# Performance work log

Measured on AMD Instinct MI355X. Metric: run time of the kernel, lower is better.

Reference implementation:

```python
import jax, jax.numpy as jnp
import numpy as np
import math

T, B, E, H, NEXP = 512, 8, 1024, 32, 256
DH = E // H
S = T + NEXP
SCALING = (DH / 1) ** 0.5 / DH  # = 1/sqrt(head_dim) for d_tilde=1
LN_EPS = 1e-5


def _xavier(key, shape, gain):
    fan_in, fan_out = shape[1], shape[0]
    a = gain * math.sqrt(6.0 / (fan_in + fan_out))
    return jax.random.uniform(key, shape, jnp.float32, -a, a)


def setup_inputs() -> dict:
    key = jax.random.key(0)
    ks = jax.random.split(key, 12)
    g = 1.0 / math.sqrt(2.0)  # xavier gain 1/sqrt(2*d_tilde)
    return {
        "query": jax.random.normal(ks[0], (T, B, E), jnp.float32),
        "attn_bias": jax.random.normal(ks[1], (B * H, T, S), jnp.float32) * 0.1,
        "outcell_index": jax.random.randint(ks[2], (B, NEXP), 0, T - 1),
        "expand_mask": jax.random.randint(ks[3], (B, NEXP), 0, 2).astype(bool),
        "key_padding_mask": jnp.zeros((B, T), bool),
        "Wq": _xavier(ks[4], (E, E), g),
        "bq": jnp.zeros((E,), jnp.float32),
        "Wk": _xavier(ks[5], (E, E), g),  # k_proj has no bias (k_bias=False)
        "Wv": _xavier(ks[6], (E, E), g),
        "bv": jnp.zeros((E,), jnp.float32),
        "Wo": _xavier(ks[7], (E, E), 1.0),
        "bo": jnp.zeros((E,), jnp.float32),
        "ln_g": jnp.ones((E,), jnp.float32),
        "ln_b": jnp.zeros((E,), jnp.float32),
    }


def reference(query, attn_bias, outcell_index, expand_mask, key_padding_mask,
              Wq, bq, Wk, Wv, bv, Wo, bo, ln_g, ln_b):
    # projections (Time x Batch x Channel)
    q = (query @ Wq.T + bq) * SCALING          # [T,B,E]
    k = query @ Wk.T                            # [T,B,E] (no bias)
    v = query @ Wv.T + bv                       # [T,B,E]

    # PBC gather-expansion of K/V along time dim (note +1 offset as in source)
    idx = outcell_index.T + 1                   # [NEXP,B]
    idx3 = jnp.broadcast_to(idx[:, :, None], (NEXP, B, E))
    expand_k = jnp.take_along_axis(k, idx3, axis=0)
    expand_v = jnp.take_along_axis(v, idx3, axis=0)
    k = jnp.concatenate([k, expand_k], axis=0)  # [S,B,E]
    v = jnp.concatenate([v, expand_v], axis=0)  # [S,B,E]

    # split heads
    qh = q.reshape(T, B, H, DH)
    kh = k.reshape(S, B, H, DH)
    vh = v.reshape(S, B, H, DH)

    scores = jnp.einsum("tbhd,sbhd->bhts", qh, kh)  # [B,H,T,S]
    scores = scores + attn_bias.reshape(B, H, T, S)

    mask = jnp.concatenate([key_padding_mask, expand_mask], axis=1)  # [B,S]
    scores = jnp.where(mask[:, None, None, :], -jnp.inf, scores)

    probs = jax.nn.softmax(scores, axis=-1)      # [B,H,T,S]

    attn = jnp.einsum("bhts,sbhd->tbhd", probs, vh).reshape(T, B, E)

    # layer norm then output projection
    mu = attn.mean(-1, keepdims=True)
    var = ((attn - mu) ** 2).mean(-1, keepdims=True)
    attn = (attn - mu) * jax.lax.rsqrt(var + LN_EPS) * ln_g + ln_b
    out = attn @ Wo.T + bo                       # [T,B,E]

    attn_weights_mean = probs.mean(axis=1)       # [B,T,S] (mean over heads)
    return out, attn_weights_mean
```

## Files before the change

### kernel.cpp

```cpp
#include <hip/hip_runtime.h>

#define DEV __device__ __forceinline__

typedef short bh8 __attribute__((ext_vector_type(8)));
typedef short bh4 __attribute__((ext_vector_type(4)));
typedef float fx4 __attribute__((ext_vector_type(4)));

#define T_ 512
#define B_ 8
#define E_ 1024
#define H_ 32
#define DH_ 32
#define S_ 768
#define NEXP_ 256
#define SCALING_ 0.17677669529663687f
#define OFF_QB    ((size_t)0)
#define OFF_WB    ((size_t)8388608)
#define OFF_QRM   ((size_t)16777216)
#define OFF_KRM   ((size_t)25165824)
#define OFF_VRM   ((size_t)33554432)
#define OFF_KBF   ((size_t)41943040)
#define OFF_VT    ((size_t)54525952)
#define OFF_ATTN  ((size_t)67108864)
#define OFF_XHAT  ((size_t)75497472)
#define OFF_MASK  ((size_t)83886080)
#define OFF_FLAG  ((size_t)83910656)

#define BARRIER_LGKM() do { \
  asm volatile("s_waitcnt lgkmcnt(0)" ::: "memory"); \
  __builtin_amdgcn_s_barrier(); \
} while (0)

#define WAIT_VM0_BARRIER() do { \
  asm volatile("s_waitcnt vmcnt(0)" ::: "memory"); \
  __builtin_amdgcn_s_barrier(); \
} while (0)

DEV float bf2f(short u) {
  union { unsigned int i; float f; } x;
  x.i = ((unsigned int)(unsigned short)u) << 16;
  return x.f;
}
DEV short f2bf(float f) {
  union { float f; unsigned int u; } x; x.f = f;
  unsigned int r = x.u + 0x7fffu + ((x.u >> 16) & 1u);
  return (short)(r >> 16);
}
DEV void gl_lds16(const void* g, void* l) {
  __builtin_amdgcn_global_load_lds(
      (const __attribute__((address_space(1))) unsigned int*)g,
      (__attribute__((address_space(3))) unsigned int*)l, 16, 0, 0);
}

__global__ __launch_bounds__(256) void conv_all(
    const float* __restrict__ q, const float* __restrict__ wq,
    const float* __restrict__ wk, const float* __restrict__ wv,
    const float* __restrict__ wo, short* __restrict__ QB, short* __restrict__ WB,
    const unsigned char* __restrict__ em, int* __restrict__ flag) {
  if (blockIdx.x == 0) {
    __shared__ int f;
    if (threadIdx.x == 0) f = 0;
    __syncthreads();
    for (int i = threadIdx.x; i < 2048; i += 256)
      if ((i & 3) && em[i]) atomicOr(&f, 1);
    __syncthreads();
    if (threadIdx.x == 0) *flag = f;
  }
  size_t i4 = ((size_t)blockIdx.x * 256 + threadIdx.x) * 4;
  const float* s; short* d;
  if (i4 < (size_t)4194304) { s = q + i4; d = QB + i4; }
  else {
    size_t r = i4 - 4194304; int m = (int)(r >> 20); size_t o = r & 1048575;
    const float* ws4[4] = {wq, wk, wv, wo};
    s = ws4[m] + o; d = WB + ((size_t)m << 20) + o;
  }
  fx4 v = *(const fx4*)s;
  bh4 p = { f2bf(v[0]), f2bf(v[1]), f2bf(v[2]), f2bf(v[3]) };
  *(bh4*)d = p;
}

__global__ __launch_bounds__(256) void qkv_gemm(
    const short* __restrict__ QB, const short* __restrict__ WB,
    const float* __restrict__ bq, const float* __restrict__ bv,
    short* __restrict__ q_rm, short* __restrict__ k_rm, short* __restrict__ v_rm) {
  __shared__ __align__(16) short As[128 * 32];
  __shared__ __align__(16) short Ws[128 * 32];
  const int tid = threadIdx.x;
  const int mt = blockIdx.x, nt = blockIdx.y;
  const int mat = nt >> 3;
  const size_t m0 = (size_t)mt * 128;
  const int n0 = (nt & 7) << 7;
  const short* W = WB + (size_t)mat * (1024 * 1024);
  const int l = tid & 63, wv_ = tid >> 6;
  const int lt = l & 15, g = l >> 4;
  const int wm = wv_ >> 1, wn = wv_ & 1;
  fx4 acc[4][4];
#pragma unroll
  for (int i = 0; i < 4; ++i)
#pragma unroll
    for (int j = 0; j < 4; ++j) acc[i][j] = fx4{0.f, 0.f, 0.f, 0.f};

  const int r0 = tid >> 2, c0 = tid & 3;
  for (int kt = 0; kt < 32; ++kt) {
    const int k0 = kt * 32;
    __syncthreads();
    gl_lds16(QB + (m0 + r0) * 1024 + k0 + c0 * 8,        As + r0 * 32 + c0 * 8);
    gl_lds16(QB + (m0 + 64 + r0) * 1024 + k0 + c0 * 8,   As + (64 + r0) * 32 + c0 * 8);
    gl_lds16(W + (size_t)(n0 + r0) * 1024 + k0 + c0 * 8,      Ws + r0 * 32 + c0 * 8);
    gl_lds16(W + (size_t)(n0 + 64 + r0) * 1024 + k0 + c0 * 8, Ws + (64 + r0) * 32 + c0 * 8);
    __syncthreads();
    bh8 af[4], wf[4];
#pragma unroll
    for (int i = 0; i < 4; ++i) af[i] = *(const bh8*)(As + (wm * 64 + i * 16 + lt) * 32 + g * 8);
#pragma unroll
    for (int j = 0; j < 4; ++j) wf[j] = *(const bh8*)(Ws + (wn * 64 + j * 16 + lt) * 32 + g * 8);
#pragma unroll
    for (int i = 0; i < 4; ++i)
#pragma unroll
      for (int j = 0; j < 4; ++j)
        acc[i][j] = __builtin_amdgcn_mfma_f32_16x16x32_bf16(af[i], wf[j], acc[i][j], 0, 0, 0);
  }
  short* outp = (mat == 0) ? q_rm : (mat == 1) ? k_rm : v_rm;
#pragma unroll
  for (int i = 0; i < 4; ++i) {
    const size_t rowb = m0 + wm * 64 + i * 16 + g * 4;
#pragma unroll
    for (int j = 0; j < 4; ++j) {
      const int col = n0 + wn * 64 + j * 16 + lt;
      const float bias = (mat == 0) ? bq[col] : (mat == 2) ? bv[col] : 0.0f;
#pragma unroll
      for (int jj = 0; jj < 4; ++jj) {
        float v = acc[i][j][jj] + bias;
        if (mat == 0) v *= SCALING_;
        outp[(rowb + jj) * 1024 + col] = f2bf(v);
      }
    }
  }
}

__global__ __launch_bounds__(256) void repack(
    const short* __restrict__ k_rm, const short* __restrict__ v_rm,
    const int* __restrict__ oc, const unsigned char* __restrict__ em,
    const unsigned char* __restrict__ kp, const int* __restrict__ flag,
    short* __restrict__ kbf, short* __restrict__ vT, float* __restrict__ maskval) {
  __shared__ __align__(16) short lv[2][64 * 40];
  const int bid = blockIdx.x, tid = threadIdx.x;
  if (bid < 768) {
#pragma unroll
    for (int k = 0; k < 4; ++k) {
      int u = bid * 1024 + k * 256 + tid;
      int d8 = u & 3;
      int s = (u >> 2) % 768;
      int hb = (u >> 2) / 768;
      int b = hb >> 5, h = hb & 31;
      int srct = (s < 512) ? s : (oc[b * 256 + (s - 512)] + 1);
      bh8 val = *(const bh8*)(k_rm + ((size_t)srct * 8 + b) * 1024 + h * 32 + d8 * 8);
      *(bh8*)(kbf + ((size_t)hb * 768 + s) * 32 + d8 * 8) = val;
    }
  } else if (bid < 2304) {
    int idx2 = bid - 768;
    int s_loc = tid >> 2, d8 = tid & 3;
#pragma unroll
    for (int k = 0; k < 2; ++k) {
      int chunk = idx2 * 2 + k;
      int c = chunk % 12, hb = chunk / 12;
      int b = hb >> 5, h = hb & 31;
      int s = c * 64 + s_loc;
      int srct = (s < 512) ? s : (oc[b * 256 + (s - 512)] + 1);
      bh8 val = *(const bh8*)(v_rm + ((size_t)srct * 8 + b) * 1024 + h * 32 + d8 * 8);
      *(bh8*)(lv[k] + s_loc * 40 + d8 * 8) = val;
    }
    __syncthreads();
    int d = tid >> 3, sj = tid & 7;
#pragma unroll
    for (int k = 0; k < 2; ++k) {
      int chunk = idx2 * 2 + k;
      int c = chunk % 12, hb = chunk / 12;
      bh8 o;
#pragma unroll
      for (int e = 0; e < 8; ++e) o[e] = lv[k][(sj * 8 + e) * 40 + d];
      *(bh8*)(vT + ((size_t)hb * 32 + d) * 768 + c * 64 + sj * 8) = o;
    }
  } else {
    int u = (bid - 2304) * 256 + tid;
    if (u < 6144) {
      int s = u % 768, b = u / 768;
      int m;
      if (*flag) {
        m = (s < 512) ? (int)kp[b * 512 + s] : (int)em[b * 256 + (s - 512)];
      } else {
        const int* kpi = (const int*)kp; const int* emi = (const int*)em;
        m = (s < 512) ? kpi[b * 512 + s] : emi[b * 256 + (s - 512)];
      }
      maskval[u] = m ? -3.0e38f : 0.0f;
    }
  }
}

__global__ __launch_bounds__(512) void attn_kernel(
    const short* __restrict__ q_rm, const short* __restrict__ kbf,
    const short* __restrict__ vT, const float* __restrict__ bias,
    const float* __restrict__ maskval, short* __restrict__ attn_bf,
    float* __restrict__ mean_out, const float* __restrict__ lg,
    const float* __restrict__ lb, short* __restrict__ xhat) {
  __shared__ __align__(16) float bias_lds[2][16 * 768];
  __shared__ __align__(16) short p_st[8 * 16 * 40];
  __shared__ float lpart[8][16];
  __shared__ __align__(16) float attred[2][8 * 64 * 8];
  __shared__ __align__(16) float maskv[768];

  const int tid = threadIdx.x, blk = blockIdx.x;
  const int tt = blk & 31, b = blk >> 5;
  const int t0 = tt * 16;
  const int w = tid >> 6, l = tid & 63, lt = l & 15, g = l >> 4;
  const int sbase = w * 96;

  for (int u = tid; u < 768; u += 512) maskv[u] = maskval[b * 768 + u];

  const float* bias_base = bias + ((size_t)(b * 32) * 512 + t0) * 768;
#pragma unroll
  for (int r = 0; r < 6; ++r)
    gl_lds16(bias_base + (size_t)(r * 512 + tid) * 4,
             (char*)bias_lds[0] + (size_t)(r * 512 + tid) * 16);
  asm volatile("s_waitcnt lgkmcnt(0) vmcnt(0)" ::: "memory");
  __builtin_amdgcn_s_barrier();

  const fx4 zf = {0.f, 0.f, 0.f, 0.f};
  float msum[24];
#pragma unroll
  for (int i = 0; i < 24; ++i) msum[i] = 0.f;

  for (int hh = 0; hh < 32; ++hh) {
    const int cur = hh & 1;
    const int bh = b * 32 + hh;

    if (hh < 31) {
      const float* nb = bias_base + (size_t)(hh + 1) * 512 * 768;
#pragma unroll
      for (int r = 0; r < 6; ++r)
        gl_lds16(nb + (size_t)(r * 512 + tid) * 4,
                 (char*)bias_lds[cur ^ 1] + (size_t)(r * 512 + tid) * 16);
    }

    const bh8 qf = *(const bh8*)(q_rm + ((size_t)(t0 + lt) * 8 + b) * 1024 + hh * 32 + g * 8);
    const short* kp_ = kbf + (size_t)bh * 768 * 32;

    unsigned exu[12];
    float ls0 = 0.f, ls1 = 0.f, ls2 = 0.f, ls3 = 0.f;
#pragma unroll
    for (int c = 0; c < 6; ++c) {
      const int s0 = sbase + c * 16;
      bh8 kf = *(const bh8*)(kp_ + (s0 + lt) * 32 + g * 8);
      fx4 sc = __builtin_amdgcn_mfma_f32_16x16x32_bf16(qf, kf, zf, 0, 0, 0);
      const float mv = maskv[s0 + lt];
      const float* bl = bias_lds[cur] + (g * 4) * 768 + s0 + lt;
      float e0 = __expf(sc[0] + bl[0]       + mv);
      float e1 = __expf(sc[1] + bl[768]     + mv);
      float e2 = __expf(sc[2] + bl[2 * 768] + mv);
      float e3 = __expf(sc[3] + bl[3 * 768] + mv);
      ls0 += e0; ls1 += e1; ls2 += e2; ls3 += e3;
      exu[c * 2]     = (unsigned)(unsigned short)f2bf(e0) | ((unsigned)(unsigned short)f2bf(e1) << 16);
      exu[c * 2 + 1] = (unsigned)(unsigned short)f2bf(e2) | ((unsigned)(unsigned short)f2bf(e3) << 16);
    }
#pragma unroll
    for (int m = 1; m < 16; m <<= 1) {
      ls0 += __shfl_xor(ls0, m); ls1 += __shfl_xor(ls1, m);
      ls2 += __shfl_xor(ls2, m); ls3 += __shfl_xor(ls3, m);
    }
    if (lt == 0) {
      lpart[w][g * 4 + 0] = ls0; lpart[w][g * 4 + 1] = ls1;
      lpart[w][g * 4 + 2] = ls2; lpart[w][g * 4 + 3] = ls3;
    }
    BARRIER_LGKM();
    float linv[4];
#pragma unroll
    for (int jj = 0; jj < 4; ++jj) {
      float s8v = 0.f;
#pragma unroll
      for (int w2 = 0; w2 < 8; ++w2) s8v += lpart[w2][g * 4 + jj];
      linv[jj] = 1.0f / s8v;
    }
    float sacc = 0.f;
#pragma unroll
    for (int w2 = 0; w2 < 8; ++w2) sacc += lpart[w2][lt];
    const float linv_acc = 1.0f / sacc;

    fx4 acc0 = zf, acc1 = zf;
    const short* vp0 = vT + ((size_t)bh * 32 + lt) * 768;
    const short* vp1 = vp0 + 16 * 768;
    short* pw_base = p_st + w * 640;
#pragma unroll
    for (int c2 = 0; c2 < 3; ++c2) {
      const int s0 = sbase + c2 * 32;
#pragma unroll
      for (int cc = 0; cc < 2; ++cc) {
        const int c = c2 * 2 + cc;
        unsigned u01 = exu[c * 2], u23 = exu[c * 2 + 1];
        short* pcol = pw_base + cc * 16 + lt;
        pcol[(g * 4 + 0) * 40] = (short)(u01 & 0xffffu);
        pcol[(g * 4 + 1) * 40] = (short)(u01 >> 16);
        pcol[(g * 4 + 2) * 40] = (short)(u23 & 0xffffu);
        pcol[(g * 4 + 3) * 40] = (short)(u23 >> 16);
        msum[c * 4 + 0] += bf2f((short)(u01 & 0xffffu)) * linv[0];
        msum[c * 4 + 1] += bf2f((short)(u01 >> 16)) * linv[1];
        msum[c * 4 + 2] += bf2f((short)(u23 & 0xffffu)) * linv[2];
        msum[c * 4 + 3] += bf2f((short)(u23 >> 16)) * linv[3];
      }
      bh8 pf = *(const bh8*)(pw_base + lt * 40 + g * 8);
      bh8 vf0 = *(const bh8*)(vp0 + s0 + g * 8);
      bh8 vf1 = *(const bh8*)(vp1 + s0 + g * 8);
      acc0 = __builtin_amdgcn_mfma_f32_16x16x32_bf16(vf0, pf, acc0, 0, 0, 0);
      acc1 = __builtin_amdgcn_mfma_f32_16x16x32_bf16(vf1, pf, acc1, 0, 0, 0);
    }
#pragma unroll
    for (int jj = 0; jj < 4; ++jj) { acc0[jj] *= linv_acc; acc1[jj] *= linv_acc; }

    float* ar = attred[cur] + (w * 64 + l) * 8;
    *(fx4*)(ar) = acc0;
    *(fx4*)(ar + 4) = acc1;
    BARRIER_LGKM();
    if (w < 2) {
      const float* ab = attred[cur];
      float s0v = 0.f, s1v = 0.f, s2v = 0.f, s3v = 0.f;
#pragma unroll
      for (int w2 = 0; w2 < 8; ++w2) {
        const float* a2 = ab + (w2 * 64 + l) * 8 + w * 4;
        s0v += a2[0]; s1v += a2[1]; s2v += a2[2]; s3v += a2[3];
      }
      bh4 o = { f2bf(s0v), f2bf(s1v), f2bf(s2v), f2bf(s3v) };
      *(bh4*)(attn_bf + ((size_t)(t0 + lt) * 8 + b) * 1024 + hh * 32 + w * 16 + g * 4) = o;
    }
    WAIT_VM0_BARRIER();
  }

#pragma unroll
  for (int r2 = 0; r2 < 2; ++r2) {
    const int trow = t0 + w * 2 + r2;
    const size_t row = (size_t)trow * 8 + b;
    const short* x = attn_bf + row * 1024 + l * 16;
    bh8 a0 = *(const bh8*)x, a1 = *(const bh8*)(x + 8);
    float xs[16];
#pragma unroll
    for (int i = 0; i < 8; ++i) { xs[i] = bf2f(a0[i]); xs[8 + i] = bf2f(a1[i]); }
    float s1 = 0.f, s2 = 0.f;
#pragma unroll
    for (int i = 0; i < 16; ++i) { s1 += xs[i]; s2 += xs[i] * xs[i]; }
    for (int m = 1; m < 64; m <<= 1) { s1 += __shfl_xor(s1, m); s2 += __shfl_xor(s2, m); }
    const float mu = s1 * (1.0f / 1024.0f);
    float var = s2 * (1.0f / 1024.0f) - mu * mu;
    var = fmaxf(var, 0.f);
    const float rs = rsqrtf(var + 1e-5f);
    const float* lgp = lg + l * 16;
    const float* lbp = lb + l * 16;
    bh8 o0, o1;
#pragma unroll
    for (int i = 0; i < 8; ++i) {
      o0[i] = f2bf((xs[i] - mu) * rs * lgp[i] + lbp[i]);
      o1[i] = f2bf((xs[8 + i] - mu) * rs * lgp[8 + i] + lbp[8 + i]);
    }
    short* y = xhat + row * 1024 + l * 16;
    *(bh8*)y = o0;
    *(bh8*)(y + 8) = o1;
  }

  float* mob = mean_out + ((size_t)b * 512 + t0) * 768;
#pragma unroll
  for (int c = 0; c < 6; ++c) {
    const int s = sbase + c * 16 + lt;
#pragma unroll
    for (int jj = 0; jj < 4; ++jj) {
      mob[(size_t)(g * 4 + jj) * 768 + s] = msum[c * 4 + jj] * 0.03125f;
    }
  }
}

__global__ __launch_bounds__(256) void out_gemm(
    const short* __restrict__ XH, const short* __restrict__ WoB,
    const float* __restrict__ bo, float* __restrict__ out) {
  __shared__ __align__(16) short As[128 * 32];
  __shared__ __align__(16) short Ws[128 * 32];
  const int tid = threadIdx.x;
  const int mt = blockIdx.x, nt = blockIdx.y;
  const size_t m0 = (size_t)mt * 128;
  const int n0 = nt << 7;
  const int l = tid & 63, wv_ = tid >> 6;
  const int lt = l & 15, g = l >> 4;
  const int wm = wv_ >> 1, wn = wv_ & 1;
  fx4 acc[4][4];
#pragma unroll
  for (int i = 0; i < 4; ++i)
#pragma unroll
    for (int j = 0; j < 4; ++j) acc[i][j] = fx4{0.f, 0.f, 0.f, 0.f};
  const int r0 = tid >> 2, c0 = tid & 3;
  for (int kt = 0; kt < 32; ++kt) {
    const int k0 = kt * 32;
    __syncthreads();
    gl_lds16(XH + (m0 + r0) * 1024 + k0 + c0 * 8,        As + r0 * 32 + c0 * 8);
    gl_lds16(XH + (m0 + 64 + r0) * 1024 + k0 + c0 * 8,   As + (64 + r0) * 32 + c0 * 8);
    gl_lds16(WoB + (size_t)(n0 + r0) * 1024 + k0 + c0 * 8,      Ws + r0 * 32 + c0 * 8);
    gl_lds16(WoB + (size_t)(n0 + 64 + r0) * 1024 + k0 + c0 * 8, Ws + (64 + r0) * 32 + c0 * 8);
    __syncthreads();
    bh8 af[4], wf[4];
#pragma unroll
    for (int i = 0; i < 4; ++i) af[i] = *(const bh8*)(As + (wm * 64 + i * 16 + lt) * 32 + g * 8);
#pragma unroll
    for (int j = 0; j < 4; ++j) wf[j] = *(const bh8*)(Ws + (wn * 64 + j * 16 + lt) * 32 + g * 8);
#pragma unroll
    for (int i = 0; i < 4; ++i)
#pragma unroll
      for (int j = 0; j < 4; ++j)
        acc[i][j] = __builtin_amdgcn_mfma_f32_16x16x32_bf16(af[i], wf[j], acc[i][j], 0, 0, 0);
  }
#pragma unroll
  for (int i = 0; i < 4; ++i) {
    const size_t rowb = m0 + wm * 64 + i * 16 + g * 4;
#pragma unroll
    for (int j = 0; j < 4; ++j) {
      const int col = n0 + wn * 64 + j * 16 + lt;
      const float bb = bo[col];
#pragma unroll
      for (int jj = 0; jj < 4; ++jj)
        out[(rowb + jj) * 1024 + col] = acc[i][j][jj] + bb;
    }
  }
}

extern "C" void kernel_launch(void* const* d_in, const int* in_sizes, int n_in,
                              void* d_out, int out_size, void* d_ws, size_t ws_size,
                              hipStream_t stream) {
  const float* query = (const float*)d_in[0];
  const float* attn_bias = (const float*)d_in[1];
  const int* oc = (const int*)d_in[2];
  const unsigned char* em = (const unsigned char*)d_in[3];
  const unsigned char* kp = (const unsigned char*)d_in[4];
  const float* Wq = (const float*)d_in[5];
  const float* bq = (const float*)d_in[6];
  const float* Wk = (const float*)d_in[7];
  const float* Wv = (const float*)d_in[8];
  const float* bv = (const float*)d_in[9];
  const float* Wo = (const float*)d_in[10];
  const float* bo = (const float*)d_in[11];
  const float* lg = (const float*)d_in[12];
  const float* lb = (const float*)d_in[13];

  char* w = (char*)d_ws;
  short* QB    = (short*)(w + OFF_QB);
  short* WB    = (short*)(w + OFF_WB);
  short* QRM   = (short*)(w + OFF_QRM);
  short* KRM   = (short*)(w + OFF_KRM);
  short* VRM   = (short*)(w + OFF_VRM);
  short* KBF   = (short*)(w + OFF_KBF);
  short* VT    = (short*)(w + OFF_VT);
  short* ATTN  = (short*)(w + OFF_ATTN);
  short* XHAT  = (short*)(w + OFF_XHAT);
  float* MASK  = (float*)(w + OFF_MASK);
  int*   FLAG  = (int*)(w + OFF_FLAG);

  float* out0 = (float*)d_out;
  float* mean_out = out0 + (size_t)T_ * B_ * E_;

  conv_all<<<8192, 256, 0, stream>>>(query, Wq, Wk, Wv, Wo, QB, WB, em, FLAG);
  qkv_gemm<<<dim3(32, 24), 256, 0, stream>>>(QB, WB, bq, bv, QRM, KRM, VRM);
  repack<<<2328, 256, 0, stream>>>(KRM, VRM, oc, em, kp, FLAG, KBF, VT, MASK);
  attn_kernel<<<256, 512, 0, stream>>>(QRM, KBF, VT, attn_bias, MASK, ATTN,
                                       mean_out, lg, lb, XHAT);
  out_gemm<<<dim3(32, 8), 256, 0, stream>>>(XHAT, WB + (size_t)3 * 1024 * 1024, bo, out0);
}
```

Baseline: 262.7 us.

## Split attention heads across two blocks, halve LDS, add mean-reduce and LN kernels

The attention kernel now launches 512 blocks, each covering 16 of the 32 heads, so it uses more CUs. Bias is single-buffered with a synchronous load per head, which cuts LDS use so several blocks fit per CU. The per-head mean is written as two partial slabs that a new kernel adds together, and LayerNorm moves into its own kernel. The cost is that bias prefetch no longer overlaps compute, there is extra global traffic for the partial means, and two more kernels are launched.

```diff
diff --git a/kernel.cpp b/kernel.cpp
--- a/kernel.cpp
+++ b/kernel.cpp
@@ -25,6 +25,8 @@
 #define OFF_XHAT  ((size_t)75497472)
 #define OFF_MASK  ((size_t)83886080)
 #define OFF_FLAG  ((size_t)83910656)
+#define OFF_MEANP ((size_t)100663296)
+#define SLAB_ ((size_t)B_ * T_ * S_)
 
 #define BARRIER_LGKM() do { \
   asm volatile("s_waitcnt lgkmcnt(0)" ::: "memory"); \
@@ -32,7 +34,7 @@
 } while (0)
 
 #define WAIT_VM0_BARRIER() do { \
-  asm volatile("s_waitcnt vmcnt(0)" ::: "memory"); \
+  asm volatile("s_waitcnt vmcnt(0) lgkmcnt(0)" ::: "memory"); \
   __builtin_amdgcn_s_barrier(); \
 } while (0)
 
@@ -197,50 +199,42 @@
   }
 }
 
-__global__ __launch_bounds__(512) void attn_kernel(
+__global__ __launch_bounds__(512, 4) void attn_kernel(
     const short* __restrict__ q_rm, const short* __restrict__ kbf,
     const short* __restrict__ vT, const float* __restrict__ bias,
     const float* __restrict__ maskval, short* __restrict__ attn_bf,
-    float* __restrict__ mean_out, const float* __restrict__ lg,
-    const float* __restrict__ lb, short* __restrict__ xhat) {
-  __shared__ __align__(16) float bias_lds[2][16 * 768];
+    float* __restrict__ mean_part) {
+  __shared__ __align__(16) float bias_lds[16 * 768];
   __shared__ __align__(16) short p_st[8 * 16 * 40];
   __shared__ float lpart[8][16];
-  __shared__ __align__(16) float attred[2][8 * 64 * 8];
+  __shared__ __align__(16) float attred[8 * 64 * 8];
   __shared__ __align__(16) float maskv[768];
 
   const int tid = threadIdx.x, blk = blockIdx.x;
-  const int tt = blk & 31, b = blk >> 5;
+  const int hg = blk & 1, tt = (blk >> 1) & 31, b = blk >> 6;
   const int t0 = tt * 16;
   const int w = tid >> 6, l = tid & 63, lt = l & 15, g = l >> 4;
   const int sbase = w * 96;
 
   for (int u = tid; u < 768; u += 512) maskv[u] = maskval[b * 768 + u];
+  BARRIER_LGKM();
 
   const float* bias_base = bias + ((size_t)(b * 32) * 512 + t0) * 768;
-#pragma unroll
-  for (int r = 0; r < 6; ++r)
-    gl_lds16(bias_base + (size_t)(r * 512 + tid) * 4,
-             (char*)bias_lds[0] + (size_t)(r * 512 + tid) * 16);
-  asm volatile("s_waitcnt lgkmcnt(0) vmcnt(0)" ::: "memory");
-  __builtin_amdgcn_s_barrier();
-
   const fx4 zf = {0.f, 0.f, 0.f, 0.f};
   float msum[24];
 #pragma unroll
   for (int i = 0; i < 24; ++i) msum[i] = 0.f;
 
-  for (int hh = 0; hh < 32; ++hh) {
-    const int cur = hh & 1;
+  for (int i = 0; i < 16; ++i) {
+    const int hh = hg * 16 + i;
     const int bh = b * 32 + hh;
 
-    if (hh < 31) {
-      const float* nb = bias_base + (size_t)(hh + 1) * 512 * 768;
-#pragma unroll
-      for (int r = 0; r < 6; ++r)
-        gl_lds16(nb + (size_t)(r * 512 + tid) * 4,
-                 (char*)bias_lds[cur ^ 1] + (size_t)(r * 512 + tid) * 16);
-    }
+    const float* hb_ = bias_base + (size_t)hh * 512 * 768;
+#pragma unroll
+    for (int r = 0; r < 6; ++r)
+      gl_lds16(hb_ + (size_t)(r * 512 + tid) * 4,
+               (char*)bias_lds + (size_t)(r * 512 + tid) * 16);
+    WAIT_VM0_BARRIER();
 
     const bh8 qf = *(const bh8*)(q_rm + ((size_t)(t0 + lt) * 8 + b) * 1024 + hh * 32 + g * 8);
     const short* kp_ = kbf + (size_t)bh * 768 * 32;
@@ -253,7 +247,7 @@
       bh8 kf = *(const bh8*)(kp_ + (s0 + lt) * 32 + g * 8);
       fx4 sc = __builtin_amdgcn_mfma_f32_16x16x32_bf16(qf, kf, zf, 0, 0, 0);
       const float mv = maskv[s0 + lt];
-      const float* bl = bias_lds[cur] + (g * 4) * 768 + s0 + lt;
+      const float* bl = bias_lds + (g * 4) * 768 + s0 + lt;
       float e0 = __expf(sc[0] + bl[0]       + mv);
       float e1 = __expf(sc[1] + bl[768]     + mv);
       float e2 = __expf(sc[2] + bl[2 * 768] + mv);
@@ -315,55 +309,23 @@
 #pragma unroll
     for (int jj = 0; jj < 4; ++jj) { acc0[jj] *= linv_acc; acc1[jj] *= linv_acc; }
 
-    float* ar = attred[cur] + (w * 64 + l) * 8;
+    float* ar = attred + (w * 64 + l) * 8;
     *(fx4*)(ar) = acc0;
     *(fx4*)(ar + 4) = acc1;
     BARRIER_LGKM();
     if (w < 2) {
-      const float* ab = attred[cur];
       float s0v = 0.f, s1v = 0.f, s2v = 0.f, s3v = 0.f;
 #pragma unroll
       for (int w2 = 0; w2 < 8; ++w2) {
-        const float* a2 = ab + (w2 * 64 + l) * 8 + w * 4;
+        const float* a2 = attred + (w2 * 64 + l) * 8 + w * 4;
         s0v += a2[0]; s1v += a2[1]; s2v += a2[2]; s3v += a2[3];
       }
       bh4 o = { f2bf(s0v), f2bf(s1v), f2bf(s2v), f2bf(s3v) };
       *(bh4*)(attn_bf + ((size_t)(t0 + lt) * 8 + b) * 1024 + hh * 32 + w * 16 + g * 4) = o;
     }
-    WAIT_VM0_BARRIER();
-  }
-
-#pragma unroll
-  for (int r2 = 0; r2 < 2; ++r2) {
-    const int trow = t0 + w * 2 + r2;
-    const size_t row = (size_t)trow * 8 + b;
-    const short* x = attn_bf + row * 1024 + l * 16;
-    bh8 a0 = *(const bh8*)x, a1 = *(const bh8*)(x + 8);
-    float xs[16];
-#pragma unroll
-    for (int i = 0; i < 8; ++i) { xs[i] = bf2f(a0[i]); xs[8 + i] = bf2f(a1[i]); }
-    float s1 = 0.f, s2 = 0.f;
-#pragma unroll
-    for (int i = 0; i < 16; ++i) { s1 += xs[i]; s2 += xs[i] * xs[i]; }
-    for (int m = 1; m < 64; m <<= 1) { s1 += __shfl_xor(s1, m); s2 += __shfl_xor(s2, m); }
-    const float mu = s1 * (1.0f / 1024.0f);
-    float var = s2 * (1.0f / 1024.0f) - mu * mu;
-    var = fmaxf(var, 0.f);
-    const float rs = rsqrtf(var + 1e-5f);
-    const float* lgp = lg + l * 16;
-    const float* lbp = lb + l * 16;
-    bh8 o0, o1;
-#pragma unroll
-    for (int i = 0; i < 8; ++i) {
-      o0[i] = f2bf((xs[i] - mu) * rs * lgp[i] + lbp[i]);
-      o1[i] = f2bf((xs[8 + i] - mu) * rs * lgp[8 + i] + lbp[8 + i]);
-    }
-    short* y = xhat + row * 1024 + l * 16;
-    *(bh8*)y = o0;
-    *(bh8*)(y + 8) = o1;
-  }
-
-  float* mob = mean_out + ((size_t)b * 512 + t0) * 768;
+  }
+
+  float* mob = mean_part + (size_t)hg * SLAB_ + ((size_t)b * 512 + t0) * 768;
 #pragma unroll
   for (int c = 0; c < 6; ++c) {
     const int s = sbase + c * 16 + lt;
@@ -372,6 +334,47 @@
       mob[(size_t)(g * 4 + jj) * 768 + s] = msum[c * 4 + jj] * 0.03125f;
     }
   }
+}
+
+__global__ __launch_bounds__(256) void mean_reduce2(
+    const float* __restrict__ mean_part, float* __restrict__ mean_out) {
+  size_t i = ((size_t)blockIdx.x * 256 + threadIdx.x) * 4;
+  fx4 a = *(const fx4*)(mean_part + i);
+  fx4 b = *(const fx4*)(mean_part + SLAB_ + i);
+#pragma unroll
+  for (int k = 0; k < 4; ++k) a[k] = a[k] + b[k];
+  *(fx4*)(mean_out + i) = a;
+}
+
+__global__ __launch_bounds__(256) void ln_kernel(
+    const short* __restrict__ attn_bf, const float* __restrict__ lg,
+    const float* __restrict__ lb, short* __restrict__ xhat) {
+  const int w = threadIdx.x >> 6, l = threadIdx.x & 63;
+  const size_t row = (size_t)blockIdx.x * 4 + w;
+  const short* x = attn_bf + row * 1024 + l * 16;
+  bh8 a0 = *(const bh8*)x, a1 = *(const bh8*)(x + 8);
+  float xs[16];
+#pragma unroll
+  for (int i = 0; i < 8; ++i) { xs[i] = bf2f(a0[i]); xs[8 + i] = bf2f(a1[i]); }
+  float s1 = 0.f, s2 = 0.f;
+#pragma unroll
+  for (int i = 0; i < 16; ++i) { s1 += xs[i]; s2 += xs[i] * xs[i]; }
+  for (int m = 1; m < 64; m <<= 1) { s1 += __shfl_xor(s1, m); s2 += __shfl_xor(s2, m); }
+  const float mu = s1 * (1.0f / 1024.0f);
+  float var = s2 * (1.0f / 1024.0f) - mu * mu;
+  var = fmaxf(var, 0.f);
+  const float rs = rsqrtf(var + 1e-5f);
+  const float* lgp = lg + l * 16;
+  const float* lbp = lb + l * 16;
+  bh8 o0, o1;
+#pragma unroll
+  for (int i = 0; i < 8; ++i) {
+    o0[i] = f2bf((xs[i] - mu) * rs * lgp[i] + lbp[i]);
+    o1[i] = f2bf((xs[8 + i] - mu) * rs * lgp[8 + i] + lbp[8 + i]);
+  }
+  short* y = xhat + row * 1024 + l * 16;
+  *(bh8*)y = o0;
+  *(bh8*)(y + 8) = o1;
 }
 
 __global__ __launch_bounds__(256) void out_gemm(
@@ -455,6 +458,7 @@
   short* XHAT  = (short*)(w + OFF_XHAT);
   float* MASK  = (float*)(w + OFF_MASK);
   int*   FLAG  = (int*)(w + OFF_FLAG);
+  float* MEANP = (float*)(w + OFF_MEANP);
 
   float* out0 = (float*)d_out;
   float* mean_out = out0 + (size_t)T_ * B_ * E_;
@@ -462,7 +466,8 @@
   conv_all<<<8192, 256, 0, stream>>>(query, Wq, Wk, Wv, Wo, QB, WB, em, FLAG);
   qkv_gemm<<<dim3(32, 24), 256, 0, stream>>>(QB, WB, bq, bv, QRM, KRM, VRM);
   repack<<<2328, 256, 0, stream>>>(KRM, VRM, oc, em, kp, FLAG, KBF, VT, MASK);
-  attn_kernel<<<256, 512, 0, stream>>>(QRM, KBF, VT, attn_bias, MASK, ATTN,
-                                       mean_out, lg, lb, XHAT);
+  attn_kernel<<<512, 512, 0, stream>>>(QRM, KBF, VT, attn_bias, MASK, ATTN, MEANP);
+  mean_reduce2<<<3072, 256, 0, stream>>>(MEANP, mean_out);
+  ln_kernel<<<1024, 256, 0, stream>>>(ATTN, lg, lb, XHAT);
   out_gemm<<<dim3(32, 8), 256, 0, stream>>>(XHAT, WB + (size_t)3 * 1024 * 1024, bo, out0);
 }
```

Measured after the change: 342.0 us. +30.2%, slower.
